# Kernel optimization log

Hardware: AMD Instinct MI355X
Metric: run time of the kernel (lower is better)

## Reference

```python
import jax, jax.numpy as jnp
import numpy as np

N_NODES = 15
K = 5
L_IN = 1920
C_OUT = 256
L3 = L_IN - 3 * K + 3  # 1908
EPS = 1e-5


def setup_inputs() -> dict:
    key = jax.random.key(0)
    ks = jax.random.split(key, 18)
    B, E = 128, 56
    s = 0.05
    inp = {
        'X': jax.random.normal(ks[0], (B, N_NODES, L_IN), jnp.float32),
        'edge_index': jax.random.randint(ks[1], (2, E), 0, N_NODES),
        'edge_weight': jax.random.uniform(ks[2], (E,), jnp.float32),
        # grouped conv params (groups = N_NODES): per-group channels 1->16->32->1
        'conv1_w': jax.random.normal(ks[3], (16 * N_NODES, 1, K), jnp.float32) * s,
        'conv1_b': jnp.zeros((16 * N_NODES,), jnp.float32),
        'conv2_w': jax.random.normal(ks[4], (32 * N_NODES, 16, K), jnp.float32) * s,
        'conv2_b': jnp.zeros((32 * N_NODES,), jnp.float32),
        'conv3_w': jax.random.normal(ks[5], (N_NODES, 32, K), jnp.float32) * s,
        'conv3_b': jnp.zeros((N_NODES,), jnp.float32),
        # GCNConv: lin weight [out,in] + bias
        'gcn_w': jax.random.normal(ks[6], (C_OUT, L3), jnp.float32) * s,
        'gcn_b': jnp.zeros((C_OUT,), jnp.float32),
        'lin1_w': jax.random.normal(ks[7], (C_OUT, L_IN), jnp.float32) * s,
        'lin1_b': jnp.zeros((C_OUT,), jnp.float32),
        # GraphNorm params
        'gn_w': jnp.ones((C_OUT,), jnp.float32),
        'gn_b': jnp.zeros((C_OUT,), jnp.float32),
        'gn_ms': jnp.ones((C_OUT,), jnp.float32),
        'out_w': jax.random.normal(ks[8], (16, C_OUT), jnp.float32) * s,
        'out_b': jnp.zeros((16,), jnp.float32),
    }
    return inp


def _gconv(x, w, b):
    # grouped valid conv1d, NCH layout
    y = jax.lax.conv_general_dilated(
        x, w, window_strides=(1,), padding='VALID',
        dimension_numbers=('NCH', 'OIH', 'NCH'),
        feature_group_count=N_NODES)
    return y + b[None, :, None]


def _gcn(x, edge_index, edge_weight, W, b):
    # x: [B, N, L3]; batched GCNConv with shared edge structure (no per-t loop)
    src, dst = edge_index[0], edge_index[1]
    loop = jnp.arange(N_NODES)
    src = jnp.concatenate([src, loop])
    dst = jnp.concatenate([dst, loop])
    ew = jnp.concatenate([edge_weight, jnp.ones((N_NODES,), edge_weight.dtype)])
    deg = jnp.zeros((N_NODES,), ew.dtype).at[dst].add(ew)  # in-degree on target
    dinv = jnp.where(deg > 0, jax.lax.rsqrt(deg), 0.0)
    norm = dinv[src] * ew * dinv[dst]  # [E']
    xl = jnp.einsum('bnf,of->bno', x, W)  # [B, N, C_OUT]
    msg = norm[None, :, None] * xl[:, src, :]  # [B, E', C_OUT]
    out = jnp.zeros_like(xl).at[:, dst, :].add(msg)
    return out + b


def reference(X, edge_index, edge_weight, conv1_w, conv1_b, conv2_w, conv2_b,
              conv3_w, conv3_b, gcn_w, gcn_b, lin1_w, lin1_b, gn_w, gn_b,
              gn_ms, out_w, out_b):
    h = jax.nn.leaky_relu(_gconv(X, conv1_w, conv1_b), 0.01)
    h = jax.nn.leaky_relu(_gconv(h, conv2_w, conv2_b), 0.01)
    h = jax.nn.leaky_relu(_gconv(h, conv3_w, conv3_b), 0.01)  # [B, N, L3]
    T = _gcn(h, edge_index, edge_weight, gcn_w, gcn_b)  # [B, N, C_OUT]
    # GraphNorm with batch=None -> single graph over dim 0
    mean = T.mean(axis=0, keepdims=True)
    out = T - mean * gn_ms
    var = (out * out).mean(axis=0, keepdims=True)
    T = gn_w * out / jnp.sqrt(var + EPS) + gn_b
    T = jax.nn.elu(T + jnp.einsum('bnl,ol->bno', X, lin1_w) + lin1_b)
    output = T.mean(axis=1)  # global_mean_pool over nodes -> [B, C_OUT]
    class_output = output @ out_w.T + out_b  # [B, 16]
    return (output, class_output)
```

## Files before the change

kernel.cpp:

```cpp
#include <hip/hip_runtime.h>

typedef unsigned short u16;
typedef unsigned int   u32;

typedef short shortx8   __attribute__((ext_vector_type(8)));
typedef float floatx4   __attribute__((ext_vector_type(4)));
typedef float floatx16  __attribute__((ext_vector_type(16)));
typedef u32   uintx2    __attribute__((ext_vector_type(2)));
typedef u32   uintx4    __attribute__((ext_vector_type(4)));

typedef u32     u32a     __attribute__((may_alias));
typedef uintx2  uintx2a  __attribute__((may_alias));
typedef uintx4  uintx4a  __attribute__((may_alias));
typedef shortx8 shortx8a __attribute__((may_alias));

__device__ __forceinline__ u16 f2bf(float f){
  union { float f; u32 i; } v; v.f = f;
  return (u16)((v.i + 0x7fffu + ((v.i >> 16) & 1u)) >> 16);
}
__device__ __forceinline__ u16 f2bf_fast(float f){
  union { float f; u32 i; } v; v.f = f;
  return (u16)((v.i + 0x8000u) >> 16);
}
__device__ __forceinline__ u32 pack2(float lo, float hi){
  union { float f; u32 i; } a, b; a.f = lo; b.f = hi;
  return __builtin_amdgcn_perm(b.i + 0x8000u, a.i + 0x8000u, 0x07060302u);
}
__device__ __forceinline__ u32 cvtpk2(float lo, float hi){
#if __has_builtin(__builtin_amdgcn_cvt_pk_bf16_f32)
  auto pv = __builtin_amdgcn_cvt_pk_bf16_f32(lo, hi);
  if constexpr (sizeof(pv) == 4){
    u32 out; __builtin_memcpy(&out, &pv, 4); return out;
  } else {
    return pack2(lo, hi);
  }
#else
  return pack2(lo, hi);
#endif
}
__device__ __forceinline__ float lrelu(float v){ return fmaxf(v, 0.01f*v); }

__global__ void __launch_bounds__(256, 4) fused_conv(
    const float* __restrict__ X,
    const float* __restrict__ w1, const float* __restrict__ b1,
    const float* __restrict__ w2, const float* __restrict__ b2,
    const float* __restrict__ w3, const float* __restrict__ b3,
    u16* __restrict__ h3p, u16* __restrict__ Xb,
    const float* __restrict__ lw, u16* __restrict__ lwb,
    const float* __restrict__ gw, u16* __restrict__ gwp,
    float* __restrict__ xlz, float* __restrict__ l1z){
  const int tid  = threadIdx.x;
  const int node = blockIdx.z;
  const int p0   = blockIdx.x * 120;
  const int b0   = blockIdx.y * 8;

  __shared__ __attribute__((aligned(16))) u16 sPair[2][4352];
  __shared__ __attribute__((aligned(16))) u16 sW2f[2560];
  __shared__ __attribute__((aligned(16))) u16 sW3f[160];
  __shared__ __attribute__((aligned(16))) u16 sXb[8*136];
  __shared__ float sW1[80], sB1[16], sB2[32];

  {
    const int bid = blockIdx.x + 16*(blockIdx.y + 16*blockIdx.z);
    int gid = bid*256 + tid;
    if (gid < 491520){
      lwb[gid] = f2bf(lw[gid]);
      xlz[gid] = 0.f;
    } else {
      int g2 = gid - 491520;
      int row = g2 / 1920;
      int col = g2 - row*1920;
      gwp[g2] = (col < 1908) ? f2bf(gw[row*1908 + col]) : (u16)0;
      l1z[g2] = 0.f;
    }
  }

  {
    const int bls = tid >> 5, i0 = tid & 31;
    const float* xrow = X  + (size_t)((b0 + bls)*15 + node)*1920;
    u16*        xbrow = Xb + (size_t)((b0 + bls)*15 + node)*1920;
    #pragma unroll
    for (int u = 0; u < 5; ++u){
      int i = i0 + 32*u;
      if (i < 136){
        int g = p0 + i;
        float xv = (g < 1920) ? xrow[g] : 0.f;
        u16 xb = f2bf_fast(xv);
        sXb[bls*136 + i] = xb;
        if (i < 120) xbrow[g] = xb;
      }
    }
    #pragma unroll
    for (int u = 0; u < 10; ++u){
      int d = tid + 256*u;
      int j = d & 7, oc = (d >> 3) & 31, kh = (d >> 8) & 1, tap = d >> 9;
      sW2f[d] = f2bf(w2[node*2560 + (oc*16 + kh*8 + j)*5 + tap]);
    }
    if (tid < 160){
      int p = tid / 5, tp = tid - 5*p;
      int ic = (p & 3) + ((p >> 2) & 1)*8 + ((p >> 3) & 1)*16 + ((p >> 4) & 1)*4;
      sW3f[tp*32 + p] = f2bf(w3[node*160 + ic*5 + tp]);
    }
    if (tid < 80) sW1[tid] = w1[node*80 + tid];
    if (tid < 16) sB1[tid] = b1[node*16 + tid];
    if (tid < 32) sB2[tid] = b2[node*32 + tid];
    {
      const int pr = tid >> 7, idx = tid & 127;
      sPair[pr][1632 + (64 + (idx >> 5))*40 + (idx & 31)] = 0;
    }
  }
  __syncthreads();

  const int w = tid >> 6, lane = tid & 63;
  const int pw = w >> 1, ph = w & 1;
  const int m = lane & 15, quad = lane >> 4;
  const int t32 = lane & 31, kh = lane >> 5;

  shortx8 a2t[5];
  #pragma unroll
  for (int tap = 0; tap < 5; ++tap)
    a2t[tap] = *(const shortx8a*)&sW2f[((tap*2 + kh)*32 + t32)*8];

  float biasr[16];
  #pragma unroll
  for (int r = 0; r < 16; ++r)
    biasr[r] = sB2[(r&3) + 8*(r>>2) + 4*kh];

  shortx8 a3[5];
  {
    const shortx8 zv = {0,0,0,0,0,0,0,0};
    #pragma unroll
    for (int tp = 0; tp < 5; ++tp){
      shortx8 t = *(const shortx8a*)&sW3f[tp*32 + quad*8];
      a3[tp] = (m == 0) ? t : zv;
    }
  }
  const float b3v = b3[node];

  shortx8 a1h = {0,0,0,0,0,0,0,0}, a1l = {0,0,0,0,0,0,0,0};
  if (quad == 0){
    const float* wrow = sW1 + m*5;
    #pragma unroll
    for (int j = 0; j < 5; ++j){
      float wv = wrow[j];
      u16 h = f2bf(wv);
      union { u32 i; float f; } hf; hf.i = ((u32)h) << 16;
      u16 l = f2bf(wv - hf.f);
      a1h[j] = (short)h; a1l[j] = (short)l;
    }
  }
  float biasA[4];
  #pragma unroll
  for (int r = 0; r < 4; ++r) biasA[r] = sB1[quad*4 + r];

  u16* h1w = sPair[pw];
  u16* h2w = sPair[pw] + 1632;

  for (int bb = 0; bb < 4; ++bb){
    const int bl = pw + bb*2;
    const int rg = (b0 + bl)*15 + node;

    {
      const int s = tid & 127;
      if (s < 68){
        const u32* xb32 = (const u32*)sXb + bl*68;
        u32 r0 = xb32[s];
        u32 r1 = (s+1 < 68) ? xb32[s+1] : 0u;
        u32 r2 = (s+2 < 68) ? xb32[s+2] : 0u;
        u32 r3 = (s+3 < 68) ? xb32[s+3] : 0u;
        u32 r4 = (s+4 < 68) ? xb32[s+4] : 0u;
        const int te = 2*s, to = 2*s + 1;
        const int offE = (s < 34) ? te*24 + 16 : 1632 + (te - 68)*40 + 32;
        const int offO = (s < 34) ? to*24 + 16 : 1632 + (to - 68)*40 + 32;
        uintx4 ve = {r0, r1, r2, r3};
        uintx4 vo = {__builtin_amdgcn_alignbit(r1, r0, 16),
                     __builtin_amdgcn_alignbit(r2, r1, 16),
                     __builtin_amdgcn_alignbit(r3, r2, 16),
                     __builtin_amdgcn_alignbit(r4, r3, 16)};
        *(uintx4a*)(h1w + offE) = ve;
        *(uintx4a*)(h1w + offO) = vo;
      }
    }
    __syncthreads();

    #pragma unroll
    for (int tt = 0; tt < 2; ++tt){
      const int p = p0 + tt*60;

      #pragma unroll
      for (int ti = 0; ti < 3; ++ti){
        const int T = ph + 2*ti;
        if (T < 5){
          const int tr = T*16 + m;
          int row = tt*60 + tr;
          row = row > 135 ? 135 : row;
          shortx8 bfr = {0,0,0,0,0,0,0,0};
          if (quad == 0){
            const int off = (row < 68) ? row*24 + 16 : 1632 + (row - 68)*40 + 32;
            bfr = *(const shortx8a*)(h1w + off);
          }
          floatx4 acc = {biasA[0], biasA[1], biasA[2], biasA[3]};
          acc = __builtin_amdgcn_mfma_f32_16x16x32_bf16(a1l, bfr, acc, 0, 0, 0);
          acc = __builtin_amdgcn_mfma_f32_16x16x32_bf16(a1h, bfr, acc, 0, 0, 0);
          if (tr < 68){
            uintx2 pk = { cvtpk2(lrelu(acc[0]), lrelu(acc[1])),
                          cvtpk2(lrelu(acc[2]), lrelu(acc[3])) };
            *(uintx2a*)(h1w + tr*24 + quad*4) = pk;
          }
        }
      }
      __syncthreads();

      {
        const int t0 = ph*32;
        floatx16 acc;
        #pragma unroll
        for (int r = 0; r < 16; ++r) acc[r] = biasr[r];
        #pragma unroll
        for (int tap = 0; tap < 5; ++tap){
          shortx8 bfr = *(const shortx8a*)(h1w + (t0 + t32 + tap)*24 + kh*8);
          acc = __builtin_amdgcn_mfma_f32_32x32x16_bf16(a2t[tap], bfr, acc, 0, 0, 0);
        }
        u16* dst = h2w + (t0 + t32)*40 + kh*16;
        uintx4 wlo = { cvtpk2(lrelu(acc[0]),  lrelu(acc[1])),
                       cvtpk2(lrelu(acc[2]),  lrelu(acc[3])),
                       cvtpk2(lrelu(acc[4]),  lrelu(acc[5])),
                       cvtpk2(lrelu(acc[6]),  lrelu(acc[7])) };
        uintx4 whi = { cvtpk2(lrelu(acc[8]),  lrelu(acc[9])),
                       cvtpk2(lrelu(acc[10]), lrelu(acc[11])),
                       cvtpk2(lrelu(acc[12]), lrelu(acc[13])),
                       cvtpk2(lrelu(acc[14]), lrelu(acc[15])) };
        *(uintx4a*)dst       = wlo;
        *(uintx4a*)(dst + 8) = whi;
      }
      __syncthreads();

      #pragma unroll
      for (int i = 0; i < 2; ++i){
        const int nt = 2*ph + i;
        floatx4 acc3 = {0.f,0.f,0.f,0.f};
        if (lane < 16) acc3[0] = b3v;
        #pragma unroll
        for (int tp = 0; tp < 5; ++tp){
          shortx8 bfr = *(const shortx8a*)(h2w + (nt*16 + m + tp)*40 + quad*8);
          acc3 = __builtin_amdgcn_mfma_f32_16x16x32_bf16(a3[tp], bfr, acc3, 0, 0, 0);
        }
        const int tl = nt*16 + lane;
        if (lane < 16 && tl < 60){
          const int t3 = p + tl;
          float v = lrelu(acc3[0]);
          h3p[(size_t)rg*1920 + t3] = (t3 < 1908) ? f2bf_fast(v) : (u16)0;
        }
      }
    }
  }
}

__global__ void __launch_bounds__(256) gemm_nt(
    const u16* __restrict__ A0, const u16* __restrict__ B0, float* __restrict__ O0,
    const u16* __restrict__ A1, const u16* __restrict__ B1, float* __restrict__ O1,
    float* __restrict__ gZ){
  const int job = blockIdx.z >> 1, khf = blockIdx.z & 1;
  const u16* A; const u16* Bm; float* O;
  if (job == 0){ A = A0; Bm = B0; O = O0; } else { A = A1; Bm = B1; O = O1; }
  __shared__ __attribute__((aligned(16))) u16 sA[2][64*88];
  __shared__ __attribute__((aligned(16))) u16 sB[2][64*88];
  const int tid = threadIdx.x;
  if (blockIdx.x == 0 && blockIdx.y == 0 && blockIdx.z == 0){
    #pragma unroll
    for (int u = 0; u < 30; ++u) gZ[tid + 256*u] = 0.f;
  }
  const int m0 = blockIdx.x*64, n0 = blockIdx.y*64;
  const int row = tid >> 2, kc = tid & 3;
  const int w = tid >> 6, lane = tid & 63;
  const int m = lane & 15, quad = lane >> 4;
  const int mo = (w & 1)*32, no = (w >> 1)*32;
  floatx4 acc[2][2];
  #pragma unroll
  for (int i = 0; i < 2; ++i)
    #pragma unroll
    for (int j = 0; j < 2; ++j)
      #pragma unroll
      for (int r = 0; r < 4; ++r) acc[i][j][r] = 0.f;

  const u16* ap = A  + (size_t)(m0 + row)*1920 + khf*960 + kc*8;
  const u16* bp = Bm + (size_t)(n0 + row)*1920 + khf*960 + kc*8;
  uintx4 va0 = *(const uintx4a*)ap;
  uintx4 va1 = *(const uintx4a*)(ap + 32);
  uintx4 vb0 = *(const uintx4a*)bp;
  uintx4 vb1 = *(const uintx4a*)(bp + 32);
  ap += 64; bp += 64;

  for (int kt = 0; kt < 15; ++kt){
    const int c = kt & 1;
    *(uintx4a*)&sA[c][row*88 + kc*8]      = va0;
    *(uintx4a*)&sA[c][row*88 + 32 + kc*8] = va1;
    *(uintx4a*)&sB[c][row*88 + kc*8]      = vb0;
    *(uintx4a*)&sB[c][row*88 + 32 + kc*8] = vb1;
    __syncthreads();
    if (kt < 14){
      va0 = *(const uintx4a*)ap;
      va1 = *(const uintx4a*)(ap + 32);
      vb0 = *(const uintx4a*)bp;
      vb1 = *(const uintx4a*)(bp + 32);
      ap += 64; bp += 64;
    }
    #pragma unroll
    for (int ks = 0; ks < 64; ks += 32){
      const shortx8 af0 = *(const shortx8a*)&sA[c][(mo      + m)*88 + ks + quad*8];
      const shortx8 af1 = *(const shortx8a*)&sA[c][(mo + 16 + m)*88 + ks + quad*8];
      const shortx8 bf0 = *(const shortx8a*)&sB[c][(no      + m)*88 + ks + quad*8];
      const shortx8 bf1 = *(const shortx8a*)&sB[c][(no + 16 + m)*88 + ks + quad*8];
      acc[0][0] = __builtin_amdgcn_mfma_f32_16x16x32_bf16(af0, bf0, acc[0][0], 0, 0, 0);
      acc[0][1] = __builtin_amdgcn_mfma_f32_16x16x32_bf16(af0, bf1, acc[0][1], 0, 0, 0);
      acc[1][0] = __builtin_amdgcn_mfma_f32_16x16x32_bf16(af1, bf0, acc[1][0], 0, 0, 0);
      acc[1][1] = __builtin_amdgcn_mfma_f32_16x16x32_bf16(af1, bf1, acc[1][1], 0, 0, 0);
    }
  }
  #pragma unroll
  for (int mi = 0; mi < 2; ++mi)
    #pragma unroll
    for (int ni = 0; ni < 2; ++ni)
      #pragma unroll
      for (int r = 0; r < 4; ++r){
        int rr = m0 + mo + mi*16 + quad*4 + r;
        int cc = n0 + no + ni*16 + m;
        atomicAdd(&O[(size_t)rr*256 + cc], acc[mi][ni][r]);
      }
}

__global__ void __launch_bounds__(256) gcn_agg(
    const float* __restrict__ xl, const int* __restrict__ ei,
    const float* __restrict__ ew, const float* __restrict__ gcn_b,
    float* __restrict__ Tpre, float* __restrict__ gS, float* __restrict__ gS2){
  const int b = blockIdx.x, tid = threadIdx.x;
  __shared__ float sxl[15*256];
  __shared__ float s_deg[15], s_dinv[15], s_norm[71];
  __shared__ int   s_cnt[15], s_start[16], s_fill[15], s_srcl[71];
  if (tid < 15){ s_deg[tid] = 0.f; s_cnt[tid] = 0; s_fill[tid] = 0; }
  #pragma unroll
  for (int n = 0; n < 15; ++n)
    sxl[n*256 + tid] = xl[(size_t)(b*15 + n)*256 + tid];
  __syncthreads();
  int se = 0, de = 0; float we = 0.f;
  if (tid < 71){
    if (tid < 56){ se = ei[tid]; de = ei[56 + tid]; we = ew[tid]; }
    else         { se = tid - 56; de = tid - 56; we = 1.0f; }
    atomicAdd(&s_deg[de], we);
    atomicAdd(&s_cnt[de], 1);
  }
  __syncthreads();
  if (tid < 15) s_dinv[tid] = s_deg[tid] > 0.f ? rsqrtf(s_deg[tid]) : 0.f;
  if (tid == 0){
    int a = 0;
    for (int n = 0; n < 15; ++n){ s_start[n] = a; a += s_cnt[n]; }
    s_start[15] = a;
  }
  __syncthreads();
  if (tid < 71){
    float nrm = s_dinv[se]*we*s_dinv[de];
    int pos = s_start[de] + atomicAdd(&s_fill[de], 1);
    s_srcl[pos] = se; s_norm[pos] = nrm;
  }
  __syncthreads();
  const float gb = gcn_b[tid];
  for (int n = 0; n < 15; ++n){
    float acc = gb;
    const int e0 = s_start[n], e1 = s_start[n+1];
    for (int idx = e0; idx < e1; ++idx)
      acc += s_norm[idx]*sxl[s_srcl[idx]*256 + tid];
    Tpre[(size_t)(b*15 + n)*256 + tid] = acc;
    atomicAdd(&gS [n*256 + tid], acc);
    atomicAdd(&gS2[n*256 + tid], acc*acc);
  }
}

__global__ void __launch_bounds__(256) finalize_k(
    const float* __restrict__ Tpre, const float* __restrict__ l1,
    const float* __restrict__ gS, const float* __restrict__ gS2,
    const float* __restrict__ gn_ms, const float* __restrict__ gn_w,
    const float* __restrict__ gn_b, const float* __restrict__ lin1_b,
    const float* __restrict__ out_w, const float* __restrict__ out_b,
    float* __restrict__ dout){
  const int b = blockIdx.x, tid = threadIdx.x;
  __shared__ float spool[256], spart[256];
  const float gnb = gn_b[tid], lb = lin1_b[tid];
  const float gms = gn_ms[tid], gwc = gn_w[tid];
  float acc = 0.f;
  #pragma unroll
  for (int n = 0; n < 15; ++n){
    const float s  = gS [n*256 + tid];
    const float s2 = gS2[n*256 + tid];
    const float mean = s*(1.f/128.f);
    const float mo   = mean*gms;
    float var = s2*(1.f/128.f) - 2.f*mo*mean + mo*mo;
    var = fmaxf(var, 0.f);
    const float scal = gwc*rsqrtf(var + 1e-5f);
    float t = (Tpre[(size_t)(b*15 + n)*256 + tid] - mo)*scal
              + gnb + l1[(size_t)(b*15 + n)*256 + tid] + lb;
    t = t > 0.f ? t : (__expf(t) - 1.f);
    acc += t;
  }
  const float pool = acc*(1.f/15.f);
  dout[b*256 + tid] = pool;
  spool[tid] = pool;
  __syncthreads();
  const int j = tid >> 4, q = tid & 15;
  float s = 0.f;
  for (int i = 0; i < 16; ++i){
    int cc = q + i*16;
    s += spool[cc]*out_w[j*256 + cc];
  }
  spart[tid] = s;
  __syncthreads();
  if (tid < 16){
    float tot = out_b[tid];
    #pragma unroll
    for (int i = 0; i < 16; ++i) tot += spart[tid*16 + i];
    dout[32768 + b*16 + tid] = tot;
  }
}

extern "C" void kernel_launch(void* const* d_in, const int* in_sizes, int n_in,
                              void* d_out, int out_size, void* d_ws, size_t ws_size,
                              hipStream_t stream){
  (void)in_sizes; (void)n_in; (void)out_size; (void)ws_size;
  const float* X    = (const float*)d_in[0];
  const int*   ei   = (const int*)d_in[1];
  const float* ew   = (const float*)d_in[2];
  const float* w1   = (const float*)d_in[3];
  const float* b1   = (const float*)d_in[4];
  const float* w2   = (const float*)d_in[5];
  const float* b2   = (const float*)d_in[6];
  const float* w3   = (const float*)d_in[7];
  const float* b3   = (const float*)d_in[8];
  const float* gw   = (const float*)d_in[9];
  const float* gb   = (const float*)d_in[10];
  const float* lw   = (const float*)d_in[11];
  const float* lb   = (const float*)d_in[12];
  const float* gnw  = (const float*)d_in[13];
  const float* gnb  = (const float*)d_in[14];
  const float* gnms = (const float*)d_in[15];
  const float* ow   = (const float*)d_in[16];
  const float* ob   = (const float*)d_in[17];

  char* ws = (char*)d_ws;
  u16*   h3p  = (u16*)(ws + 0);
  u16*   gwp  = (u16*)(ws + 7372800);
  u16*   Xb   = (u16*)(ws + 8355840);
  u16*   lwb  = (u16*)(ws + 15728640);
  float* xl   = (float*)(ws + 16711680);
  float* l1   = (float*)(ws + 18677760);
  float* gS   = (float*)(ws + 20643840);
  float* gS2  = (float*)(ws + 20659200);
  float* Tpre = (float*)(ws + 0);

  fused_conv<<<dim3(16, 16, 15), dim3(256), 0, stream>>>(X, w1, b1, w2, b2, w3, b3,
                                                         h3p, Xb, lw, lwb, gw, gwp,
                                                         xl, l1);
  gemm_nt   <<<dim3(30, 4, 4),   dim3(256), 0, stream>>>(Xb, lwb, l1, h3p, gwp, xl, gS);
  gcn_agg   <<<dim3(128),        dim3(256), 0, stream>>>(xl, ei, ew, gb, Tpre, gS, gS2);
  finalize_k<<<dim3(128),        dim3(256), 0, stream>>>(Tpre, l1, gS, gS2,
                                                         gnms, gnw, gnb, lb, ow, ob,
                                                         (float*)d_out);
}
```

Before: 195.1 us.

## Fold the X·lin1 GEMM into the conv kernel as an extra grid slice

Adds a z=0 slice to the conv launch that computes the X·lin1ᵀ GEMM directly from fp32 inputs, converting them to bf16 in registers. It no longer writes the bf16 copies of X and lin1_w, and no longer zeroes the l1 buffer. The later gemm_nt launch now handles only the GCN projection, with half as many blocks. The goal is to cut global traffic and run the lin1 GEMM alongside the conv work. The cost is a GEMM with a single split-K pass and no double buffering, running 30 k-steps in one block, plus fp32 loads that are twice as wide.

```diff
diff --git a/kernel.cpp b/kernel.cpp
--- a/kernel.cpp
+++ b/kernel.cpp
@@ -13,6 +13,7 @@
 typedef uintx2  uintx2a  __attribute__((may_alias));
 typedef uintx4  uintx4a  __attribute__((may_alias));
 typedef shortx8 shortx8a __attribute__((may_alias));
+typedef floatx4 floatx4a __attribute__((may_alias));
 
 __device__ __forceinline__ u16 f2bf(float f){
   union { float f; u32 i; } v; v.f = f;
@@ -40,73 +41,153 @@
 }
 __device__ __forceinline__ float lrelu(float v){ return fmaxf(v, 0.01f*v); }
 
-__global__ void __launch_bounds__(256, 4) fused_conv(
+struct ConvSmem {
+  u16 sPair[2][4352];
+  u16 sW2f[2560];
+  u16 sW3f[160];
+  u16 sXb[8*136];
+  float sW1[80];
+  float sB1[16];
+  float sB2[32];
+};
+struct GemmSmem {
+  u16 sA[64*88];
+  u16 sB[64*88];
+};
+
+__global__ void __launch_bounds__(256, 4) conv_gemm0(
     const float* __restrict__ X,
     const float* __restrict__ w1, const float* __restrict__ b1,
     const float* __restrict__ w2, const float* __restrict__ b2,
     const float* __restrict__ w3, const float* __restrict__ b3,
-    u16* __restrict__ h3p, u16* __restrict__ Xb,
-    const float* __restrict__ lw, u16* __restrict__ lwb,
-    const float* __restrict__ gw, u16* __restrict__ gwp,
-    float* __restrict__ xlz, float* __restrict__ l1z){
-  const int tid  = threadIdx.x;
-  const int node = blockIdx.z;
+    u16* __restrict__ h3p,
+    const float* __restrict__ lw, const float* __restrict__ gw,
+    u16* __restrict__ gwp, float* __restrict__ xlz, float* __restrict__ l1o){
+  __shared__ __attribute__((aligned(16))) char sMem[25536];
+  const int tid = threadIdx.x;
+
+  if (blockIdx.z == 0){
+    const int l = blockIdx.x + 16*blockIdx.y;
+    if (l >= 120) return;
+    GemmSmem& gs = *reinterpret_cast<GemmSmem*>(sMem);
+    const int m0 = (l >> 2)*64, n0 = (l & 3)*64;
+    const int row = tid >> 2, kc = tid & 3;
+    const int w = tid >> 6, lane = tid & 63;
+    const int m = lane & 15, quad = lane >> 4;
+    const int mo = (w & 1)*32, no = (w >> 1)*32;
+    floatx4 acc[2][2];
+    #pragma unroll
+    for (int i = 0; i < 2; ++i)
+      #pragma unroll
+      for (int j = 0; j < 2; ++j)
+        #pragma unroll
+        for (int r = 0; r < 4; ++r) acc[i][j][r] = 0.f;
+
+    const float* apf = X  + (size_t)(m0 + row)*1920 + kc*16;
+    const float* bpf = lw + (size_t)(n0 + row)*1920 + kc*16;
+    floatx4 va[4], vb[4];
+    #pragma unroll
+    for (int q = 0; q < 4; ++q){
+      va[q] = *(const floatx4a*)(apf + 4*q);
+      vb[q] = *(const floatx4a*)(bpf + 4*q);
+    }
+    apf += 64; bpf += 64;
+
+    for (int kt = 0; kt < 30; ++kt){
+      uintx4 wa0 = { cvtpk2(va[0][0],va[0][1]), cvtpk2(va[0][2],va[0][3]),
+                     cvtpk2(va[1][0],va[1][1]), cvtpk2(va[1][2],va[1][3]) };
+      uintx4 wa1 = { cvtpk2(va[2][0],va[2][1]), cvtpk2(va[2][2],va[2][3]),
+                     cvtpk2(va[3][0],va[3][1]), cvtpk2(va[3][2],va[3][3]) };
+      uintx4 wb0 = { cvtpk2(vb[0][0],vb[0][1]), cvtpk2(vb[0][2],vb[0][3]),
+                     cvtpk2(vb[1][0],vb[1][1]), cvtpk2(vb[1][2],vb[1][3]) };
+      uintx4 wb1 = { cvtpk2(vb[2][0],vb[2][1]), cvtpk2(vb[2][2],vb[2][3]),
+                     cvtpk2(vb[3][0],vb[3][1]), cvtpk2(vb[3][2],vb[3][3]) };
+      *(uintx4a*)&gs.sA[row*88 + kc*16]     = wa0;
+      *(uintx4a*)&gs.sA[row*88 + kc*16 + 8] = wa1;
+      *(uintx4a*)&gs.sB[row*88 + kc*16]     = wb0;
+      *(uintx4a*)&gs.sB[row*88 + kc*16 + 8] = wb1;
+      __syncthreads();
+      if (kt < 29){
+        #pragma unroll
+        for (int q = 0; q < 4; ++q){
+          va[q] = *(const floatx4a*)(apf + 4*q);
+          vb[q] = *(const floatx4a*)(bpf + 4*q);
+        }
+        apf += 64; bpf += 64;
+      }
+      #pragma unroll
+      for (int ks = 0; ks < 64; ks += 32){
+        const shortx8 af0 = *(const shortx8a*)&gs.sA[(mo      + m)*88 + ks + quad*8];
+        const shortx8 af1 = *(const shortx8a*)&gs.sA[(mo + 16 + m)*88 + ks + quad*8];
+        const shortx8 bf0 = *(const shortx8a*)&gs.sB[(no      + m)*88 + ks + quad*8];
+        const shortx8 bf1 = *(const shortx8a*)&gs.sB[(no + 16 + m)*88 + ks + quad*8];
+        acc[0][0] = __builtin_amdgcn_mfma_f32_16x16x32_bf16(af0, bf0, acc[0][0], 0, 0, 0);
+        acc[0][1] = __builtin_amdgcn_mfma_f32_16x16x32_bf16(af0, bf1, acc[0][1], 0, 0, 0);
+        acc[1][0] = __builtin_amdgcn_mfma_f32_16x16x32_bf16(af1, bf0, acc[1][0], 0, 0, 0);
+        acc[1][1] = __builtin_amdgcn_mfma_f32_16x16x32_bf16(af1, bf1, acc[1][1], 0, 0, 0);
+      }
+      __syncthreads();
+    }
+    #pragma unroll
+    for (int mi = 0; mi < 2; ++mi)
+      #pragma unroll
+      for (int ni = 0; ni < 2; ++ni)
+        #pragma unroll
+        for (int r = 0; r < 4; ++r){
+          int rr = m0 + mo + mi*16 + quad*4 + r;
+          int cc = n0 + no + ni*16 + m;
+          l1o[(size_t)rr*256 + cc] = acc[mi][ni][r];
+        }
+    return;
+  }
+
+  ConvSmem& cs = *reinterpret_cast<ConvSmem*>(sMem);
+  const int node = blockIdx.z - 1;
   const int p0   = blockIdx.x * 120;
   const int b0   = blockIdx.y * 8;
 
-  __shared__ __attribute__((aligned(16))) u16 sPair[2][4352];
-  __shared__ __attribute__((aligned(16))) u16 sW2f[2560];
-  __shared__ __attribute__((aligned(16))) u16 sW3f[160];
-  __shared__ __attribute__((aligned(16))) u16 sXb[8*136];
-  __shared__ float sW1[80], sB1[16], sB2[32];
-
   {
-    const int bid = blockIdx.x + 16*(blockIdx.y + 16*blockIdx.z);
+    const int bid = blockIdx.x + 16*(blockIdx.y + 16*node);
     int gid = bid*256 + tid;
     if (gid < 491520){
-      lwb[gid] = f2bf(lw[gid]);
       xlz[gid] = 0.f;
     } else {
       int g2 = gid - 491520;
       int row = g2 / 1920;
       int col = g2 - row*1920;
       gwp[g2] = (col < 1908) ? f2bf(gw[row*1908 + col]) : (u16)0;
-      l1z[g2] = 0.f;
     }
   }
 
   {
     const int bls = tid >> 5, i0 = tid & 31;
-    const float* xrow = X  + (size_t)((b0 + bls)*15 + node)*1920;
-    u16*        xbrow = Xb + (size_t)((b0 + bls)*15 + node)*1920;
+    const float* xrow = X + (size_t)((b0 + bls)*15 + node)*1920;
     #pragma unroll
     for (int u = 0; u < 5; ++u){
       int i = i0 + 32*u;
       if (i < 136){
         int g = p0 + i;
         float xv = (g < 1920) ? xrow[g] : 0.f;
-        u16 xb = f2bf_fast(xv);
-        sXb[bls*136 + i] = xb;
-        if (i < 120) xbrow[g] = xb;
+        cs.sXb[bls*136 + i] = f2bf_fast(xv);
       }
     }
     #pragma unroll
     for (int u = 0; u < 10; ++u){
       int d = tid + 256*u;
       int j = d & 7, oc = (d >> 3) & 31, kh = (d >> 8) & 1, tap = d >> 9;
-      sW2f[d] = f2bf(w2[node*2560 + (oc*16 + kh*8 + j)*5 + tap]);
+      cs.sW2f[d] = f2bf(w2[node*2560 + (oc*16 + kh*8 + j)*5 + tap]);
     }
     if (tid < 160){
       int p = tid / 5, tp = tid - 5*p;
       int ic = (p & 3) + ((p >> 2) & 1)*8 + ((p >> 3) & 1)*16 + ((p >> 4) & 1)*4;
-      sW3f[tp*32 + p] = f2bf(w3[node*160 + ic*5 + tp]);
-    }
-    if (tid < 80) sW1[tid] = w1[node*80 + tid];
-    if (tid < 16) sB1[tid] = b1[node*16 + tid];
-    if (tid < 32) sB2[tid] = b2[node*32 + tid];
+      cs.sW3f[tp*32 + p] = f2bf(w3[node*160 + ic*5 + tp]);
+    }
+    if (tid < 80) cs.sW1[tid] = w1[node*80 + tid];
+    if (tid < 16) cs.sB1[tid] = b1[node*16 + tid];
+    if (tid < 32) cs.sB2[tid] = b2[node*32 + tid];
     {
       const int pr = tid >> 7, idx = tid & 127;
-      sPair[pr][1632 + (64 + (idx >> 5))*40 + (idx & 31)] = 0;
+      cs.sPair[pr][1632 + (64 + (idx >> 5))*40 + (idx & 31)] = 0;
     }
   }
   __syncthreads();
@@ -119,19 +200,19 @@
   shortx8 a2t[5];
   #pragma unroll
   for (int tap = 0; tap < 5; ++tap)
-    a2t[tap] = *(const shortx8a*)&sW2f[((tap*2 + kh)*32 + t32)*8];
+    a2t[tap] = *(const shortx8a*)&cs.sW2f[((tap*2 + kh)*32 + t32)*8];
 
   float biasr[16];
   #pragma unroll
   for (int r = 0; r < 16; ++r)
-    biasr[r] = sB2[(r&3) + 8*(r>>2) + 4*kh];
+    biasr[r] = cs.sB2[(r&3) + 8*(r>>2) + 4*kh];
 
   shortx8 a3[5];
   {
     const shortx8 zv = {0,0,0,0,0,0,0,0};
     #pragma unroll
     for (int tp = 0; tp < 5; ++tp){
-      shortx8 t = *(const shortx8a*)&sW3f[tp*32 + quad*8];
+      shortx8 t = *(const shortx8a*)&cs.sW3f[tp*32 + quad*8];
       a3[tp] = (m == 0) ? t : zv;
     }
   }
@@ -139,22 +220,22 @@
 
   shortx8 a1h = {0,0,0,0,0,0,0,0}, a1l = {0,0,0,0,0,0,0,0};
   if (quad == 0){
-    const float* wrow = sW1 + m*5;
+    const float* wrow = cs.sW1 + m*5;
     #pragma unroll
     for (int j = 0; j < 5; ++j){
       float wv = wrow[j];
       u16 h = f2bf(wv);
       union { u32 i; float f; } hf; hf.i = ((u32)h) << 16;
-      u16 l = f2bf(wv - hf.f);
-      a1h[j] = (short)h; a1l[j] = (short)l;
+      u16 lo = f2bf(wv - hf.f);
+      a1h[j] = (short)h; a1l[j] = (short)lo;
     }
   }
   float biasA[4];
   #pragma unroll
-  for (int r = 0; r < 4; ++r) biasA[r] = sB1[quad*4 + r];
-
-  u16* h1w = sPair[pw];
-  u16* h2w = sPair[pw] + 1632;
+  for (int r = 0; r < 4; ++r) biasA[r] = cs.sB1[quad*4 + r];
+
+  u16* h1w = cs.sPair[pw];
+  u16* h2w = cs.sPair[pw] + 1632;
 
   for (int bb = 0; bb < 4; ++bb){
     const int bl = pw + bb*2;
@@ -163,7 +244,7 @@
     {
       const int s = tid & 127;
       if (s < 68){
-        const u32* xb32 = (const u32*)sXb + bl*68;
+        const u32* xb32 = (const u32*)cs.sXb + bl*68;
         u32 r0 = xb32[s];
         u32 r1 = (s+1 < 68) ? xb32[s+1] : 0u;
         u32 r2 = (s+2 < 68) ? xb32[s+2] : 0u;
@@ -257,12 +338,9 @@
 }
 
 __global__ void __launch_bounds__(256) gemm_nt(
-    const u16* __restrict__ A0, const u16* __restrict__ B0, float* __restrict__ O0,
-    const u16* __restrict__ A1, const u16* __restrict__ B1, float* __restrict__ O1,
-    float* __restrict__ gZ){
-  const int job = blockIdx.z >> 1, khf = blockIdx.z & 1;
-  const u16* A; const u16* Bm; float* O;
-  if (job == 0){ A = A0; Bm = B0; O = O0; } else { A = A1; Bm = B1; O = O1; }
+    const u16* __restrict__ A, const u16* __restrict__ Bm,
+    float* __restrict__ O, float* __restrict__ gZ){
+  const int khf = blockIdx.z;
   __shared__ __attribute__((aligned(16))) u16 sA[2][64*88];
   __shared__ __attribute__((aligned(16))) u16 sB[2][64*88];
   const int tid = threadIdx.x;
@@ -447,18 +525,15 @@
   char* ws = (char*)d_ws;
   u16*   h3p  = (u16*)(ws + 0);
   u16*   gwp  = (u16*)(ws + 7372800);
-  u16*   Xb   = (u16*)(ws + 8355840);
-  u16*   lwb  = (u16*)(ws + 15728640);
   float* xl   = (float*)(ws + 16711680);
   float* l1   = (float*)(ws + 18677760);
   float* gS   = (float*)(ws + 20643840);
   float* gS2  = (float*)(ws + 20659200);
   float* Tpre = (float*)(ws + 0);
 
-  fused_conv<<<dim3(16, 16, 15), dim3(256), 0, stream>>>(X, w1, b1, w2, b2, w3, b3,
-                                                         h3p, Xb, lw, lwb, gw, gwp,
-                                                         xl, l1);
-  gemm_nt   <<<dim3(30, 4, 4),   dim3(256), 0, stream>>>(Xb, lwb, l1, h3p, gwp, xl, gS);
+  conv_gemm0<<<dim3(16, 16, 16), dim3(256), 0, stream>>>(X, w1, b1, w2, b2, w3, b3,
+                                                         h3p, lw, gw, gwp, xl, l1);
+  gemm_nt   <<<dim3(30, 4, 2),   dim3(256), 0, stream>>>(h3p, gwp, xl, gS);
   gcn_agg   <<<dim3(128),        dim3(256), 0, stream>>>(xl, ei, ew, gb, Tpre, gS, gS2);
   finalize_k<<<dim3(128),        dim3(256), 0, stream>>>(Tpre, l1, gS, gS2,
                                                          gnms, gnw, gnb, lb, ow, ob,
```

Result: no change. 196.6 us (+0.8%).
